# Kernel optimization log

Hardware: AMD Instinct MI355X
Metric: run time of the kernel (lower is better)

The kernel has to match this reference:

```python
import jax, jax.numpy as jnp
import numpy as np

B, H, W, C = 2, 64, 64, 96
DIN, NST, RNK, K = 192, 16, 6, 4
L = H * W


def _make_ids():
    idx = np.arange(L).reshape(H, W)
    p0 = idx.reshape(-1)
    p1 = idx.T.reshape(-1)
    p2 = p0[::-1].copy()
    p3 = p1[::-1].copy()
    scan = np.stack([p0, p1, p2, p3]).astype(np.int32)
    inv = np.stack([np.argsort(p) for p in scan]).astype(np.int32)
    return jnp.asarray(scan), jnp.asarray(inv)


def setup_inputs() -> dict:
    key = jax.random.key(0)
    ks = jax.random.split(key, 10)
    scan_ids, inv_ids = _make_ids()
    std = RNK ** -0.5
    # dt bias init: inverse-softplus of dt ~ LogUniform(1e-3, 1e-1), as in VMM.dt_init
    u = jax.random.uniform(ks[5], (K, DIN))
    dt = jnp.exp(u * (np.log(0.1) - np.log(0.001)) + np.log(0.001))
    dt_b = dt + jnp.log(-jnp.expm1(-dt))
    return {
        "x": jax.random.normal(ks[0], (B, H, W, C), jnp.float32),
        "W_in": jax.random.normal(ks[1], (2 * DIN, C), jnp.float32) * 0.02,
        "conv_w": jax.random.normal(ks[2], (DIN, 1, 3, 3), jnp.float32) * 0.1,
        "conv_b": jnp.zeros((DIN,), jnp.float32),
        "x_proj_w": jax.random.normal(ks[3], (K, RNK + 2 * NST, DIN), jnp.float32) * 0.02,
        "dt_w": jax.random.uniform(ks[4], (K, DIN, RNK), jnp.float32, -std, std),
        "dt_b": dt_b.astype(jnp.float32),
        "A_logs": jnp.log(jnp.tile(jnp.arange(1, NST + 1, dtype=jnp.float32)[None], (K * DIN, 1))),
        "Ds": jnp.ones((K * DIN,), jnp.float32),
        "gate_w": jax.random.normal(ks[6], (4 * DIN, 4), jnp.float32) * 0.1,  # grouped 1x1 conv, groups=DIN
        "gate_b": jnp.zeros((4 * DIN,), jnp.float32),
        "ln_g": jnp.ones((DIN,), jnp.float32),
        "ln_b": jnp.zeros((DIN,), jnp.float32),
        "W_out": jax.random.normal(ks[7], (C, DIN), jnp.float32) * 0.02,
        "scan_ids": scan_ids,
        "inv_ids": inv_ids,
    }


def _forward(x, W_in, conv_w, conv_b, x_proj_w, dt_w, dt_b, A_logs, Ds, gate_w, gate_b, ln_g, ln_b, W_out, scan_ids, inv_ids):
    b, h, w, c = x.shape
    l = h * w
    din = conv_w.shape[0]
    k = x_proj_w.shape[0]
    nst = A_logs.shape[1]
    rnk = dt_w.shape[2]
    # in_proj + split into x / gate z
    xz = x @ W_in.T
    xc, z = jnp.split(xz, 2, axis=-1)
    xc = jnp.transpose(xc, (0, 3, 1, 2))  # (b, din, h, w)
    # depthwise 3x3 conv + SiLU
    xc = jax.lax.conv_general_dilated(
        xc, conv_w, (1, 1), "SAME", feature_group_count=din,
        dimension_numbers=("NCHW", "OIHW", "NCHW")) + conv_b[None, :, None, None]
    xc = jax.nn.silu(xc)
    # multi-directional gather (mair_ids_scan)
    xf = xc.reshape(b, din, l)
    xs = jnp.moveaxis(xf[:, :, scan_ids], 2, 1)  # (b, k, din, l)
    # x_proj (grouped 1x1 conv) -> dt, B, C
    x_dbl = jnp.einsum("bkdl,krd->bkrl", xs, x_proj_w)
    dts, Bs, Cs = jnp.split(x_dbl, [rnk, rnk + nst], axis=2)  # (b,k,rnk,l),(b,k,n,l),(b,k,n,l)
    delta = jax.nn.softplus(jnp.einsum("bkrl,kdr->bkdl", dts, dt_w) + dt_b[None, :, :, None])
    A = -jnp.exp(A_logs).reshape(k, din, nst)
    dA = jnp.exp(delta[..., None] * A[None, :, :, None, :])              # (b,k,d,l,n)
    dBu = (delta * xs)[..., None] * jnp.moveaxis(Bs, 2, 3)[:, :, None]   # (b,k,d,l,n)

    def step(hst, inp):
        da, dbu = inp
        hst = da * hst + dbu
        return hst, hst

    h0 = jnp.zeros((b, k, din, nst), jnp.float32)
    _, hs = jax.lax.scan(step, h0, (jnp.moveaxis(dA, 3, 0), jnp.moveaxis(dBu, 3, 0)))  # (l,b,k,d,n)
    ys = jnp.einsum("lbkdn,bknl->bkdl", hs, Cs) + xs * Ds.reshape(k, din)[None, :, :, None]
    # inverse scatter (mair_ids_inverse) + concat along channels
    y = jax.vmap(lambda yk, ik: yk[..., ik], in_axes=(1, 0), out_axes=1)(ys, inv_ids)
    y = y.reshape(b, k * din, h, w)
    # ShuffleAttn gating: group = din, group_channels = k
    shuf = y.reshape(b, k, din, h, w).transpose(0, 2, 1, 3, 4).reshape(b, k * din, h, w)
    pooled = shuf.mean(axis=(2, 3)).reshape(b, din, k)
    gate = jax.nn.sigmoid(jnp.einsum("bgi,goi->bgo", pooled, gate_w.reshape(din, k, k)) + gate_b.reshape(din, k))
    gate = gate.transpose(0, 2, 1).reshape(b, k * din)  # channel_rearrange
    y = y * gate[:, :, None, None]
    # sum the 4 direction branches
    y = y.reshape(b, k, din, h, w).sum(axis=1)
    y = jnp.transpose(y, (0, 2, 3, 1))  # (b,h,w,din)
    # LayerNorm(d_inner)
    mu = y.mean(-1, keepdims=True)
    var = ((y - mu) ** 2).mean(-1, keepdims=True)
    y = (y - mu) / jnp.sqrt(var + 1e-5) * ln_g + ln_b
    y = y * jax.nn.silu(z)
    return y @ W_out.T


def reference(x, W_in, conv_w, conv_b, x_proj_w, dt_w, dt_b, A_logs, Ds, gate_w, gate_b, ln_g, ln_b, W_out, scan_ids, inv_ids):
    return _forward(x, W_in, conv_w, conv_b, x_proj_w, dt_w, dt_b, A_logs, Ds, gate_w, gate_b, ln_g, ln_b, W_out, scan_ids, inv_ids)
```

## Files before the change

kernel.cpp:

```cpp
#include <hip/hip_runtime.h>
#include <math.h>

#define BB 2
#define CC 96
#define DIN 192
#define NST 16
#define RNK 6
#define KK 4
#define LL 4096
#define RTOT (RNK + 2*NST)


__global__ __launch_bounds__(256) void k_inproj(const float* __restrict__ x,
        const float* __restrict__ W_in, float* __restrict__ xc_pre,
        float* __restrict__ z_silu) {
    __shared__ float lx[96*65];
    __shared__ float wt[48*196];
    int b = blockIdx.y, z = blockIdx.z;
    int l0 = blockIdx.x * 64;
    int t = threadIdx.x;
    for (int i = 0; i < 24; ++i) {
        int e = t + 256*i;
        int l = e / 96, c = e % 96;
        lx[c*65 + l] = x[((size_t)(b*LL + l0 + l))*96 + c];
    }
    int lg = t & 15;
    int og = t >> 4;
    float acc[4][12];
    #pragma unroll
    for (int j = 0; j < 4; ++j)
        #pragma unroll
        for (int q = 0; q < 12; ++q) acc[j][q] = 0.f;
    for (int p = 0; p < 2; ++p) {
        __syncthreads();
        for (int i = 0; i < 36; ++i) {
            int e = t + 256*i;
            int cc = e % 48, oc = e / 48;
            wt[cc*196 + oc] = W_in[((size_t)(z*192 + oc))*96 + p*48 + cc];
        }
        __syncthreads();
        #pragma unroll 2
        for (int cc = 0; cc < 48; ++cc) {
            int c = p*48 + cc;
            float x0 = lx[c*65 + 4*lg + 0];
            float x1 = lx[c*65 + 4*lg + 1];
            float x2 = lx[c*65 + 4*lg + 2];
            float x3 = lx[c*65 + 4*lg + 3];
            const float* wr = &wt[cc*196 + 12*og];
            float4 w0 = *(const float4*)(wr);
            float4 w1 = *(const float4*)(wr + 4);
            float4 w2 = *(const float4*)(wr + 8);
            float wv[12] = {w0.x,w0.y,w0.z,w0.w, w1.x,w1.y,w1.z,w1.w,
                            w2.x,w2.y,w2.z,w2.w};
            #pragma unroll
            for (int q = 0; q < 12; ++q) {
                acc[0][q] += x0*wv[q];
                acc[1][q] += x1*wv[q];
                acc[2][q] += x2*wv[q];
                acc[3][q] += x3*wv[q];
            }
        }
    }
    float* dst = (z == 0) ? xc_pre : z_silu;
    #pragma unroll
    for (int j = 0; j < 4; ++j) {
        int l = l0 + 4*lg + j;
        size_t base = (size_t)(b*LL + l)*DIN + 12*og;
        #pragma unroll
        for (int q = 0; q < 12; ++q) {
            float v = acc[j][q];
            if (z) v = v / (1.f + __expf(-v));
            dst[base + q] = v;
        }
    }
}

__global__ __launch_bounds__(256) void k_conv(const float* __restrict__ xc,
        const float* __restrict__ cw, const float* __restrict__ cb,
        float* __restrict__ out) {
    int gid = blockIdx.x*256 + threadIdx.x;
    int d = gid % DIN;
    int r = gid / DIN;
    int l = r & 4095, b = r >> 12;
    int w = l & 63, h = l >> 6;
    float acc = cb[d];
    #pragma unroll
    for (int dh = -1; dh <= 1; ++dh) {
        int h2 = h + dh;
        bool okh = (h2 >= 0) && (h2 < 64);
        #pragma unroll
        for (int dw = -1; dw <= 1; ++dw) {
            int w2 = w + dw;
            if (okh && w2 >= 0 && w2 < 64)
                acc += xc[((size_t)(b*LL + h2*64 + w2))*DIN + d] * cw[d*9 + (dh+1)*3 + (dw+1)];
        }
    }
    out[((size_t)(b*LL + l))*DIN + d] = acc / (1.f + __expf(-acc));
}

__global__ __launch_bounds__(512) void k_proj(const float* __restrict__ xconv,
        const int* __restrict__ scan_ids,
        const float* __restrict__ xpw, const float* __restrict__ dtw,
        const float* __restrict__ dtb,
        float* __restrict__ Bs, float* __restrict__ Cs, float* __restrict__ delta) {
    __shared__ float lxs[DIN*65];
    __shared__ float lw[RTOT*DIN];
    __shared__ float lbc[64*33];
    __shared__ float ldts[RNK*64];
    __shared__ int lsid[64];
    int k = blockIdx.y, b = blockIdx.z;
    int l0 = blockIdx.x * 64;
    int t = threadIdx.x;
    if (t < 64) lsid[t] = scan_ids[k*LL + l0 + t];
    for (int i = 0; i < 15; ++i) {
        int e = t + 512*i;
        if (e < RTOT*DIN) lw[e] = xpw[(size_t)k*RTOT*DIN + e];
    }
    __syncthreads();
    for (int i = 0; i < 24; ++i) {
        int e = t + 512*i;
        int d = e % DIN, l = e / DIN;
        lxs[d*65 + l] = xconv[((size_t)(b*LL + lsid[l]))*DIN + d];
    }
    __syncthreads();
    int l = t & 63;
    int rg = __builtin_amdgcn_readfirstlane(t >> 6);
    float acc[5];
    #pragma unroll
    for (int j = 0; j < 5; ++j) acc[j] = 0.f;
    for (int d = 0; d < DIN; d += 4) {
        float x0 = lxs[(d+0)*65 + l];
        float x1 = lxs[(d+1)*65 + l];
        float x2 = lxs[(d+2)*65 + l];
        float x3 = lxs[(d+3)*65 + l];
        #pragma unroll
        for (int j = 0; j < 5; ++j) {
            int r = rg + 8*j;
            if (r < RTOT) {
                float4 w = *(const float4*)&lw[r*DIN + d];
                acc[j] += x0*w.x + x1*w.y + x2*w.z + x3*w.w;
            }
        }
    }
    #pragma unroll
    for (int j = 0; j < 5; ++j) {
        int r = rg + 8*j;
        if (r < RTOT) {
            if (r < RNK) ldts[r*64 + l] = acc[j];
            else         lbc[l*33 + (r - RNK)] = acc[j];
        }
    }
    __syncthreads();
    size_t rowb = ((size_t)((b*KK + k)*LL + l0))*NST;
    for (int i = 0; i < 2; ++i) {
        int e = t + 512*i;
        int n = e & 15, ll = e >> 4;
        Bs[rowb + ll*NST + n] = lbc[ll*33 + n];
        Cs[rowb + ll*NST + n] = lbc[ll*33 + 16 + n];
    }
    for (int i = 0; i < 24; ++i) {
        int e = t + 512*i;
        int d = e % DIN, ll = e / DIN;
        float a = dtb[k*DIN + d];
        #pragma unroll
        for (int r = 0; r < RNK; ++r)
            a += ldts[r*64 + ll] * dtw[(k*DIN + d)*RNK + r];
        float sp = fmaxf(a, 0.f) + __logf(1.f + __expf(-fabsf(a)));
        delta[((size_t)((b*KK + k)*LL + l0 + ll))*DIN + d] = sp;
    }
}

__global__ __launch_bounds__(192) void k_scan1(const float* __restrict__ delta,
        const float* __restrict__ xconv, const float* __restrict__ Bs,
        const int* __restrict__ scan_ids, const float* __restrict__ A_logs,
        float* __restrict__ segA, float* __restrict__ segB, int SL) {
    __shared__ int lsid[256];
    int seg = blockIdx.x, bk = blockIdx.y;
    int b = bk >> 2, k = bk & 3;
    int d = threadIdx.x;
    int l0 = seg * SL;
    for (int i = threadIdx.x; i < SL; i += 192) lsid[i] = scan_ids[k*LL + l0 + i];
    __syncthreads();
    float Av[16];
    {
        const float4* ap = (const float4*)(A_logs + (k*DIN + d)*NST);
        #pragma unroll
        for (int q = 0; q < 4; ++q) {
            float4 v = ap[q];
            Av[4*q+0] = -__expf(v.x); Av[4*q+1] = -__expf(v.y);
            Av[4*q+2] = -__expf(v.z); Av[4*q+3] = -__expf(v.w);
        }
    }
    float a[16], h[16];
    #pragma unroll
    for (int n = 0; n < 16; ++n) { a[n] = 1.f; h[n] = 0.f; }
    const float* dp = delta + ((size_t)bk*LL + l0)*DIN + d;
    const float4* bq = (const float4*)(Bs + ((size_t)bk*LL + l0)*NST);
    for (int li = 0; li < SL; ++li) {
        float dv = dp[(size_t)li*DIN];
        float xv = xconv[((size_t)(b*LL + lsid[li]))*DIN + d];
        float dxv = dv * xv;
        float bb[16];
        #pragma unroll
        for (int q = 0; q < 4; ++q) {
            float4 v = bq[li*4 + q];
            bb[4*q+0] = v.x; bb[4*q+1] = v.y; bb[4*q+2] = v.z; bb[4*q+3] = v.w;
        }
        #pragma unroll
        for (int n = 0; n < 16; ++n) {
            float e = __expf(dv * Av[n]);
            a[n] *= e;
            h[n] = e*h[n] + dxv*bb[n];
        }
    }
    float4* sa = (float4*)(segA + (((size_t)bk*gridDim.x + seg)*DIN + d)*NST);
    float4* sb = (float4*)(segB + (((size_t)bk*gridDim.x + seg)*DIN + d)*NST);
    #pragma unroll
    for (int q = 0; q < 4; ++q) {
        sa[q] = make_float4(a[4*q], a[4*q+1], a[4*q+2], a[4*q+3]);
        sb[q] = make_float4(h[4*q], h[4*q+1], h[4*q+2], h[4*q+3]);
    }
}

__global__ __launch_bounds__(256) void k_scan2(const float* __restrict__ segA,
        const float* __restrict__ segB, float* __restrict__ hinit, int SEGC) {
    int idx = blockIdx.x*256 + threadIdx.x;
    if (idx >= BB*KK*DIN*NST) return;
    int bk = idx / (DIN*NST);
    int dn = idx % (DIN*NST);
    float h = 0.f;
    for (int s = 0; s < SEGC; ++s) {
        size_t o = ((size_t)(bk*SEGC + s))*(DIN*NST) + dn;
        hinit[o] = h;
        h = segA[o]*h + segB[o];
    }
}

__global__ __launch_bounds__(192) void k_scan3(const float* __restrict__ delta,
        const float* __restrict__ xconv, const float* __restrict__ Bs,
        const float* __restrict__ Cs,
        const int* __restrict__ scan_ids, const float* __restrict__ A_logs,
        const float* __restrict__ Ds, const float* __restrict__ hinit,
        float* __restrict__ y_dirs, float* __restrict__ poolsum, int SL) {
    __shared__ int lsid[256];
    int seg = blockIdx.x, bk = blockIdx.y;
    int b = bk >> 2, k = bk & 3;
    int d = threadIdx.x;
    int l0 = seg * SL;
    for (int i = threadIdx.x; i < SL; i += 192) lsid[i] = scan_ids[k*LL + l0 + i];
    __syncthreads();
    float Av[16];
    {
        const float4* ap = (const float4*)(A_logs + (k*DIN + d)*NST);
        #pragma unroll
        for (int q = 0; q < 4; ++q) {
            float4 v = ap[q];
            Av[4*q+0] = -__expf(v.x); Av[4*q+1] = -__expf(v.y);
            Av[4*q+2] = -__expf(v.z); Av[4*q+3] = -__expf(v.w);
        }
    }
    float Dv = Ds[k*DIN + d];
    float h[16];
    {
        const float4* hp = (const float4*)(hinit + (((size_t)bk*gridDim.x + seg)*DIN + d)*NST);
        #pragma unroll
        for (int q = 0; q < 4; ++q) {
            float4 v = hp[q];
            h[4*q+0] = v.x; h[4*q+1] = v.y; h[4*q+2] = v.z; h[4*q+3] = v.w;
        }
    }
    const float* dp = delta + ((size_t)bk*LL + l0)*DIN + d;
    const float4* bq = (const float4*)(Bs + ((size_t)bk*LL + l0)*NST);
    const float4* cq = (const float4*)(Cs + ((size_t)bk*LL + l0)*NST);
    float pool = 0.f;
    for (int li = 0; li < SL; ++li) {
        float dv = dp[(size_t)li*DIN];
        int l = lsid[li];
        float xv = xconv[((size_t)(b*LL + l))*DIN + d];
        float dxv = dv * xv;
        float bb[16], cc[16];
        #pragma unroll
        for (int q = 0; q < 4; ++q) {
            float4 v = bq[li*4 + q];
            bb[4*q+0] = v.x; bb[4*q+1] = v.y; bb[4*q+2] = v.z; bb[4*q+3] = v.w;
            float4 u = cq[li*4 + q];
            cc[4*q+0] = u.x; cc[4*q+1] = u.y; cc[4*q+2] = u.z; cc[4*q+3] = u.w;
        }
        float y = 0.f;
        #pragma unroll
        for (int n = 0; n < 16; ++n) {
            float e = __expf(dv * Av[n]);
            h[n] = e*h[n] + dxv*bb[n];
            y += h[n]*cc[n];
        }
        y += xv * Dv;
        y_dirs[((size_t)(bk*LL + l))*DIN + d] = y;
        pool += y;
    }
    atomicAdd(&poolsum[(b*DIN + d)*KK + k], pool);
}

__global__ void k_gate(const float* __restrict__ poolsum, const float* __restrict__ gw,
        const float* __restrict__ gb, float* __restrict__ gate) {
    int idx = blockIdx.x*256 + threadIdx.x;
    int o = idx & 3;
    int bd = idx >> 2;
    int d = bd % DIN;
    float acc = gb[d*KK + o];
    #pragma unroll
    for (int i = 0; i < KK; ++i)
        acc += (poolsum[bd*KK + i] * (1.f/LL)) * gw[(d*KK + o)*KK + i];
    gate[idx] = 1.f/(1.f + __expf(-acc));
}

__global__ __launch_bounds__(256) void k_final(const float* __restrict__ y_dirs,
        const float* __restrict__ gate, const float* __restrict__ z_silu,
        const float* __restrict__ lng, const float* __restrict__ lnb,
        const float* __restrict__ Wout, float* __restrict__ out) {
    __shared__ float buf[16*193];
    __shared__ float lmu[16], lrs[16];
    int b = blockIdx.y;
    int l0 = blockIdx.x * 16;
    int t = threadIdx.x;
    for (int i = 0; i < 12; ++i) {
        int e = t + 256*i;
        int d = e % DIN, l = e / DIN;
        float acc = 0.f;
        #pragma unroll
        for (int k = 0; k < KK; ++k)
            acc += y_dirs[((size_t)((b*KK + k)*LL + l0 + l))*DIN + d] * gate[(b*DIN + d)*KK + k];
        buf[l*193 + d] = acc;
    }
    __syncthreads();
    int l2 = t >> 4, q = t & 15;
    float s = 0.f, s2 = 0.f;
    for (int i = 0; i < 12; ++i) {
        float v = buf[l2*193 + q + 16*i];
        s += v; s2 += v*v;
    }
    s += __shfl_xor(s, 1);  s2 += __shfl_xor(s2, 1);
    s += __shfl_xor(s, 2);  s2 += __shfl_xor(s2, 2);
    s += __shfl_xor(s, 4);  s2 += __shfl_xor(s2, 4);
    s += __shfl_xor(s, 8);  s2 += __shfl_xor(s2, 8);
    if (q == 0) {
        float mu = s * (1.f/DIN);
        float var = s2 * (1.f/DIN) - mu*mu;
        lmu[l2] = mu;
        lrs[l2] = rsqrtf(var + 1e-5f);
    }
    __syncthreads();
    for (int i = 0; i < 12; ++i) {
        int e = t + 256*i;
        int d = e % DIN, l = e / DIN;
        float v = buf[l*193 + d];
        float tv = (v - lmu[l]) * lrs[l] * lng[d] + lnb[d];
        tv *= z_silu[((size_t)(b*LL + l0 + l))*DIN + d];
        buf[l*193 + d] = tv;
    }
    __syncthreads();
    int l = t & 15;
    int c0 = (t >> 4) * 6;
    float acc[6];
    #pragma unroll
    for (int cc = 0; cc < 6; ++cc) acc[cc] = 0.f;
    for (int d = 0; d < DIN; ++d) {
        float v = buf[l*193 + d];
        #pragma unroll
        for (int cc = 0; cc < 6; ++cc)
            acc[cc] += v * Wout[(c0 + cc)*DIN + d];
    }
    #pragma unroll
    for (int cc = 0; cc < 6; ++cc)
        out[((size_t)(b*LL + l0 + l))*CC + c0 + cc] = acc[cc];
}

extern "C" void kernel_launch(void* const* d_in, const int* in_sizes, int n_in,
                              void* d_out, int out_size, void* d_ws, size_t ws_size,
                              hipStream_t stream) {
    const float* x      = (const float*)d_in[0];
    const float* W_in   = (const float*)d_in[1];
    const float* conv_w = (const float*)d_in[2];
    const float* conv_b = (const float*)d_in[3];
    const float* xpw    = (const float*)d_in[4];
    const float* dt_w   = (const float*)d_in[5];
    const float* dt_b   = (const float*)d_in[6];
    const float* A_logs = (const float*)d_in[7];
    const float* Ds     = (const float*)d_in[8];
    const float* gate_w = (const float*)d_in[9];
    const float* gate_b = (const float*)d_in[10];
    const float* ln_g   = (const float*)d_in[11];
    const float* ln_b   = (const float*)d_in[12];
    const float* W_out  = (const float*)d_in[13];
    const int* scan_ids = (const int*)d_in[14];
    float* out = (float*)d_out;

    const size_t baseF = 6291456ull  + 2ull*1572864
                       + 6291456ull  + 2ull*524288  + 3072;
    int SEGC = 16;
    if ((baseF + 3ull*128*24576)*4 <= ws_size) SEGC = 128;
    else if ((baseF + 3ull*64*24576)*4 <= ws_size) SEGC = 64;
    else if ((baseF + 3ull*32*24576)*4 <= ws_size) SEGC = 32;
    int SL = LL / SEGC;
    size_t segF = (size_t)SEGC * 24576;

    float* ws      = (float*)d_ws;
    float* y_dirs  = ws;
    float* xc_pre  = ws;
    float* z_silu  = y_dirs  + 6291456;
    float* xconv   = z_silu  + 1572864;
    float* delta   = xconv   + 1572864;
    float* Bs      = delta   + 6291456;
    float* Cs      = Bs      + 524288;
    float* poolsum = Cs      + 524288;
    float* gate    = poolsum + 1536;
    float* segA    = gate    + 1536;
    float* segB    = segA    + segF;
    float* hinit   = segB    + segF;

    hipMemsetAsync(poolsum, 0, 1536*sizeof(float), stream);

    k_inproj<<<dim3(LL/64, BB, 2), 256, 0, stream>>>(x, W_in, xc_pre, z_silu);
    k_conv<<<(BB*DIN*LL)/256, 256, 0, stream>>>(xc_pre, conv_w, conv_b, xconv);
    k_proj<<<dim3(LL/64, KK, BB), 512, 0, stream>>>(xconv, scan_ids, xpw, dt_w, dt_b,
                                                    Bs, Cs, delta);
    k_scan1<<<dim3(SEGC, BB*KK), 192, 0, stream>>>(delta, xconv, Bs, scan_ids,
                                                   A_logs, segA, segB, SL);
    k_scan2<<<(BB*KK*DIN*NST + 255)/256, 256, 0, stream>>>(segA, segB, hinit, SEGC);
    k_scan3<<<dim3(SEGC, BB*KK), 192, 0, stream>>>(delta, xconv, Bs, Cs, scan_ids,
                                                   A_logs, Ds, hinit, y_dirs, poolsum, SL);
    k_gate<<<(BB*DIN*KK)/256, 256, 0, stream>>>(poolsum, gate_w, gate_b, gate);
    k_final<<<dim3(LL/16, BB), 256, 0, stream>>>(y_dirs, gate, z_silu, ln_g, ln_b, W_out, out);
}
```

Measured before the change: 319.5 us.

## Fuse dt projection into scan kernels and split state dim across thread pairs

k_proj now writes only the low-rank dt values (6 per position), and k_scan1/k_scan3 recompute delta = softplus(dt_w·dts + b) per 32-step chunk into shared memory. This removes the large delta tensor and its write and re-read traffic. Each scan thread now handles 8 of the 16 state channels, using 384 threads per block, and the halves of y are combined with a shuffle. B/C are staged in LDS, xconv is prefetched one step ahead, and k_proj's LDS is halved by looping over two DIN halves. The cost is computing delta twice, once in each scan pass, and extra barriers per chunk.

```diff
diff --git a/kernel.cpp b/kernel.cpp
--- a/kernel.cpp
+++ b/kernel.cpp
@@ -99,127 +99,133 @@
 }
 
 __global__ __launch_bounds__(512) void k_proj(const float* __restrict__ xconv,
-        const int* __restrict__ scan_ids,
-        const float* __restrict__ xpw, const float* __restrict__ dtw,
-        const float* __restrict__ dtb,
-        float* __restrict__ Bs, float* __restrict__ Cs, float* __restrict__ delta) {
-    __shared__ float lxs[DIN*65];
-    __shared__ float lw[RTOT*DIN];
+        const int* __restrict__ scan_ids, const float* __restrict__ xpw,
+        float* __restrict__ dts, float* __restrict__ Bs, float* __restrict__ Cs) {
+    __shared__ float lxs[96*65];
+    __shared__ float lw[RTOT*96];
     __shared__ float lbc[64*33];
-    __shared__ float ldts[RNK*64];
     __shared__ int lsid[64];
     int k = blockIdx.y, b = blockIdx.z;
     int l0 = blockIdx.x * 64;
     int t = threadIdx.x;
     if (t < 64) lsid[t] = scan_ids[k*LL + l0 + t];
-    for (int i = 0; i < 15; ++i) {
-        int e = t + 512*i;
-        if (e < RTOT*DIN) lw[e] = xpw[(size_t)k*RTOT*DIN + e];
-    }
-    __syncthreads();
-    for (int i = 0; i < 24; ++i) {
-        int e = t + 512*i;
-        int d = e % DIN, l = e / DIN;
-        lxs[d*65 + l] = xconv[((size_t)(b*LL + lsid[l]))*DIN + d];
-    }
-    __syncthreads();
     int l = t & 63;
     int rg = __builtin_amdgcn_readfirstlane(t >> 6);
     float acc[5];
     #pragma unroll
     for (int j = 0; j < 5; ++j) acc[j] = 0.f;
-    for (int d = 0; d < DIN; d += 4) {
-        float x0 = lxs[(d+0)*65 + l];
-        float x1 = lxs[(d+1)*65 + l];
-        float x2 = lxs[(d+2)*65 + l];
-        float x3 = lxs[(d+3)*65 + l];
-        #pragma unroll
-        for (int j = 0; j < 5; ++j) {
-            int r = rg + 8*j;
-            if (r < RTOT) {
-                float4 w = *(const float4*)&lw[r*DIN + d];
-                acc[j] += x0*w.x + x1*w.y + x2*w.z + x3*w.w;
-            }
-        }
-    }
+    for (int p = 0; p < 2; ++p) {
+        __syncthreads();
+        for (int i = 0; i < 12; ++i) {
+            int e = t + 512*i;
+            int dd = e % 96, ll = e / 96;
+            lxs[dd*65 + ll] = xconv[((size_t)(b*LL + lsid[ll]))*DIN + p*96 + dd];
+        }
+        for (int i = 0; i < 8; ++i) {
+            int e = t + 512*i;
+            if (e < RTOT*96) {
+                int r = e / 96, dd = e % 96;
+                lw[r*96 + dd] = xpw[(size_t)k*RTOT*DIN + r*DIN + p*96 + dd];
+            }
+        }
+        __syncthreads();
+        for (int dd = 0; dd < 96; dd += 4) {
+            float x0 = lxs[(dd+0)*65 + l];
+            float x1 = lxs[(dd+1)*65 + l];
+            float x2 = lxs[(dd+2)*65 + l];
+            float x3 = lxs[(dd+3)*65 + l];
+            #pragma unroll
+            for (int j = 0; j < 5; ++j) {
+                int r = rg + 8*j;
+                if (r < RTOT) {
+                    float4 w = *(const float4*)&lw[r*96 + dd];
+                    acc[j] += x0*w.x + x1*w.y + x2*w.z + x3*w.w;
+                }
+            }
+        }
+    }
+    int bk = b*KK + k;
     #pragma unroll
     for (int j = 0; j < 5; ++j) {
         int r = rg + 8*j;
-        if (r < RTOT) {
-            if (r < RNK) ldts[r*64 + l] = acc[j];
-            else         lbc[l*33 + (r - RNK)] = acc[j];
-        }
-    }
-    __syncthreads();
-    size_t rowb = ((size_t)((b*KK + k)*LL + l0))*NST;
+        if (r < RNK)       dts[((size_t)bk*LL + l0 + l)*8 + r] = acc[j];
+        else if (r < RTOT) lbc[l*33 + (r - RNK)] = acc[j];
+    }
+    __syncthreads();
+    size_t rowb = ((size_t)bk*LL + l0)*NST;
     for (int i = 0; i < 2; ++i) {
         int e = t + 512*i;
         int n = e & 15, ll = e >> 4;
         Bs[rowb + ll*NST + n] = lbc[ll*33 + n];
         Cs[rowb + ll*NST + n] = lbc[ll*33 + 16 + n];
     }
-    for (int i = 0; i < 24; ++i) {
-        int e = t + 512*i;
-        int d = e % DIN, ll = e / DIN;
-        float a = dtb[k*DIN + d];
-        #pragma unroll
-        for (int r = 0; r < RNK; ++r)
-            a += ldts[r*64 + ll] * dtw[(k*DIN + d)*RNK + r];
-        float sp = fmaxf(a, 0.f) + __logf(1.f + __expf(-fabsf(a)));
-        delta[((size_t)((b*KK + k)*LL + l0 + ll))*DIN + d] = sp;
-    }
-}
-
-__global__ __launch_bounds__(192) void k_scan1(const float* __restrict__ delta,
-        const float* __restrict__ xconv, const float* __restrict__ Bs,
+}
+
+__global__ __launch_bounds__(384) void k_scan1(const float* __restrict__ xconv,
+        const float* __restrict__ Bs, const float* __restrict__ dts,
+        const float* __restrict__ dtw, const float* __restrict__ dtb,
         const int* __restrict__ scan_ids, const float* __restrict__ A_logs,
         float* __restrict__ segA, float* __restrict__ segB, int SL) {
+    __shared__ float ldel[32*DIN];
+    __shared__ float lB[32*NST];
     __shared__ int lsid[256];
     int seg = blockIdx.x, bk = blockIdx.y;
     int b = bk >> 2, k = bk & 3;
-    int d = threadIdx.x;
+    int t = threadIdx.x;
+    int half = t & 1, d = t >> 1;
     int l0 = seg * SL;
-    for (int i = threadIdx.x; i < SL; i += 192) lsid[i] = scan_ids[k*LL + l0 + i];
-    __syncthreads();
-    float Av[16];
+    for (int i = t; i < SL; i += 384) lsid[i] = scan_ids[k*LL + l0 + i];
+    float Av[8];
     {
-        const float4* ap = (const float4*)(A_logs + (k*DIN + d)*NST);
-        #pragma unroll
-        for (int q = 0; q < 4; ++q) {
-            float4 v = ap[q];
-            Av[4*q+0] = -__expf(v.x); Av[4*q+1] = -__expf(v.y);
-            Av[4*q+2] = -__expf(v.z); Av[4*q+3] = -__expf(v.w);
-        }
-    }
-    float a[16], h[16];
-    #pragma unroll
-    for (int n = 0; n < 16; ++n) { a[n] = 1.f; h[n] = 0.f; }
-    const float* dp = delta + ((size_t)bk*LL + l0)*DIN + d;
-    const float4* bq = (const float4*)(Bs + ((size_t)bk*LL + l0)*NST);
-    for (int li = 0; li < SL; ++li) {
-        float dv = dp[(size_t)li*DIN];
-        float xv = xconv[((size_t)(b*LL + lsid[li]))*DIN + d];
-        float dxv = dv * xv;
-        float bb[16];
-        #pragma unroll
-        for (int q = 0; q < 4; ++q) {
-            float4 v = bq[li*4 + q];
-            bb[4*q+0] = v.x; bb[4*q+1] = v.y; bb[4*q+2] = v.z; bb[4*q+3] = v.w;
-        }
-        #pragma unroll
-        for (int n = 0; n < 16; ++n) {
-            float e = __expf(dv * Av[n]);
-            a[n] *= e;
-            h[n] = e*h[n] + dxv*bb[n];
-        }
-    }
-    float4* sa = (float4*)(segA + (((size_t)bk*gridDim.x + seg)*DIN + d)*NST);
-    float4* sb = (float4*)(segB + (((size_t)bk*gridDim.x + seg)*DIN + d)*NST);
-    #pragma unroll
-    for (int q = 0; q < 4; ++q) {
-        sa[q] = make_float4(a[4*q], a[4*q+1], a[4*q+2], a[4*q+3]);
-        sb[q] = make_float4(h[4*q], h[4*q+1], h[4*q+2], h[4*q+3]);
-    }
+        const float4* ap = (const float4*)(A_logs + ((k*DIN + d)*NST + half*8));
+        float4 a0 = ap[0], a1 = ap[1];
+        Av[0]=-__expf(a0.x); Av[1]=-__expf(a0.y); Av[2]=-__expf(a0.z); Av[3]=-__expf(a0.w);
+        Av[4]=-__expf(a1.x); Av[5]=-__expf(a1.y); Av[6]=-__expf(a1.z); Av[7]=-__expf(a1.w);
+    }
+    int dd = t % DIN, li0 = t / DIN;
+    float wdt[RNK];
+    float bdt = dtb[k*DIN + dd];
+    #pragma unroll
+    for (int r = 0; r < RNK; ++r) wdt[r] = dtw[(k*DIN + dd)*RNK + r];
+    float a[8], h[8];
+    #pragma unroll
+    for (int n = 0; n < 8; ++n) { a[n] = 1.f; h[n] = 0.f; }
+    __syncthreads();
+    float xn = xconv[((size_t)(b*LL + lsid[0]))*DIN + d];
+    for (int c0 = 0; c0 < SL; c0 += 32) {
+        for (int li = li0; li < 32; li += 2) {
+            const float* dr = dts + ((size_t)bk*LL + l0 + c0 + li)*8;
+            float aa = bdt;
+            #pragma unroll
+            for (int r = 0; r < RNK; ++r) aa += dr[r]*wdt[r];
+            ldel[li*DIN + dd] = fmaxf(aa, 0.f) + __logf(1.f + __expf(-fabsf(aa)));
+        }
+        for (int e = t; e < 32*NST; e += 384)
+            lB[e] = Bs[((size_t)bk*LL + l0 + c0)*NST + e];
+        __syncthreads();
+        for (int li2 = 0; li2 < 32; ++li2) {
+            int li = c0 + li2;
+            float xv = xn;
+            if (li + 1 < SL) xn = xconv[((size_t)(b*LL + lsid[li+1]))*DIN + d];
+            float dv = ldel[li2*DIN + d];
+            float dxv = dv * xv;
+            float4 b0 = *(const float4*)&lB[li2*NST + half*8];
+            float4 b1 = *(const float4*)&lB[li2*NST + half*8 + 4];
+            float bb[8] = {b0.x,b0.y,b0.z,b0.w, b1.x,b1.y,b1.z,b1.w};
+            #pragma unroll
+            for (int n = 0; n < 8; ++n) {
+                float e2 = __expf(dv * Av[n]);
+                a[n] *= e2;
+                h[n] = e2*h[n] + dxv*bb[n];
+            }
+        }
+        __syncthreads();
+    }
+    size_t base = (((size_t)bk*gridDim.x + seg)*DIN + d)*NST + half*8;
+    *(float4*)&segA[base]     = make_float4(a[0],a[1],a[2],a[3]);
+    *(float4*)&segA[base + 4] = make_float4(a[4],a[5],a[6],a[7]);
+    *(float4*)&segB[base]     = make_float4(h[0],h[1],h[2],h[3]);
+    *(float4*)&segB[base + 4] = make_float4(h[4],h[5],h[6],h[7]);
 }
 
 __global__ __launch_bounds__(256) void k_scan2(const float* __restrict__ segA,
@@ -229,6 +235,7 @@
     int bk = idx / (DIN*NST);
     int dn = idx % (DIN*NST);
     float h = 0.f;
+    #pragma unroll 4
     for (int s = 0; s < SEGC; ++s) {
         size_t o = ((size_t)(bk*SEGC + s))*(DIN*NST) + dn;
         hinit[o] = h;
@@ -236,68 +243,90 @@
     }
 }
 
-__global__ __launch_bounds__(192) void k_scan3(const float* __restrict__ delta,
-        const float* __restrict__ xconv, const float* __restrict__ Bs,
-        const float* __restrict__ Cs,
+__global__ __launch_bounds__(384) void k_scan3(const float* __restrict__ xconv,
+        const float* __restrict__ Bs, const float* __restrict__ Cs,
+        const float* __restrict__ dts, const float* __restrict__ dtw,
+        const float* __restrict__ dtb,
         const int* __restrict__ scan_ids, const float* __restrict__ A_logs,
         const float* __restrict__ Ds, const float* __restrict__ hinit,
         float* __restrict__ y_dirs, float* __restrict__ poolsum, int SL) {
+    __shared__ float ldel[32*DIN];
+    __shared__ float lB[32*NST];
+    __shared__ float lC[32*NST];
     __shared__ int lsid[256];
     int seg = blockIdx.x, bk = blockIdx.y;
     int b = bk >> 2, k = bk & 3;
-    int d = threadIdx.x;
+    int t = threadIdx.x;
+    int half = t & 1, d = t >> 1;
     int l0 = seg * SL;
-    for (int i = threadIdx.x; i < SL; i += 192) lsid[i] = scan_ids[k*LL + l0 + i];
-    __syncthreads();
-    float Av[16];
+    for (int i = t; i < SL; i += 384) lsid[i] = scan_ids[k*LL + l0 + i];
+    float Av[8];
     {
-        const float4* ap = (const float4*)(A_logs + (k*DIN + d)*NST);
-        #pragma unroll
-        for (int q = 0; q < 4; ++q) {
-            float4 v = ap[q];
-            Av[4*q+0] = -__expf(v.x); Av[4*q+1] = -__expf(v.y);
-            Av[4*q+2] = -__expf(v.z); Av[4*q+3] = -__expf(v.w);
-        }
+        const float4* ap = (const float4*)(A_logs + ((k*DIN + d)*NST + half*8));
+        float4 a0 = ap[0], a1 = ap[1];
+        Av[0]=-__expf(a0.x); Av[1]=-__expf(a0.y); Av[2]=-__expf(a0.z); Av[3]=-__expf(a0.w);
+        Av[4]=-__expf(a1.x); Av[5]=-__expf(a1.y); Av[6]=-__expf(a1.z); Av[7]=-__expf(a1.w);
     }
     float Dv = Ds[k*DIN + d];
-    float h[16];
+    int dd = t % DIN, li0 = t / DIN;
+    float wdt[RNK];
+    float bdt = dtb[k*DIN + dd];
+    #pragma unroll
+    for (int r = 0; r < RNK; ++r) wdt[r] = dtw[(k*DIN + dd)*RNK + r];
+    float h[8];
     {
-        const float4* hp = (const float4*)(hinit + (((size_t)bk*gridDim.x + seg)*DIN + d)*NST);
-        #pragma unroll
-        for (int q = 0; q < 4; ++q) {
-            float4 v = hp[q];
-            h[4*q+0] = v.x; h[4*q+1] = v.y; h[4*q+2] = v.z; h[4*q+3] = v.w;
-        }
-    }
-    const float* dp = delta + ((size_t)bk*LL + l0)*DIN + d;
-    const float4* bq = (const float4*)(Bs + ((size_t)bk*LL + l0)*NST);
-    const float4* cq = (const float4*)(Cs + ((size_t)bk*LL + l0)*NST);
+        size_t base = (((size_t)bk*gridDim.x + seg)*DIN + d)*NST + half*8;
+        float4 h0 = *(const float4*)&hinit[base];
+        float4 h1 = *(const float4*)&hinit[base + 4];
+        h[0]=h0.x; h[1]=h0.y; h[2]=h0.z; h[3]=h0.w;
+        h[4]=h1.x; h[5]=h1.y; h[6]=h1.z; h[7]=h1.w;
+    }
+    __syncthreads();
+    float xn = xconv[((size_t)(b*LL + lsid[0]))*DIN + d];
     float pool = 0.f;
-    for (int li = 0; li < SL; ++li) {
-        float dv = dp[(size_t)li*DIN];
-        int l = lsid[li];
-        float xv = xconv[((size_t)(b*LL + l))*DIN + d];
-        float dxv = dv * xv;
-        float bb[16], cc[16];
-        #pragma unroll
-        for (int q = 0; q < 4; ++q) {
-            float4 v = bq[li*4 + q];
-            bb[4*q+0] = v.x; bb[4*q+1] = v.y; bb[4*q+2] = v.z; bb[4*q+3] = v.w;
-            float4 u = cq[li*4 + q];
-            cc[4*q+0] = u.x; cc[4*q+1] = u.y; cc[4*q+2] = u.z; cc[4*q+3] = u.w;
-        }
-        float y = 0.f;
-        #pragma unroll
-        for (int n = 0; n < 16; ++n) {
-            float e = __expf(dv * Av[n]);
-            h[n] = e*h[n] + dxv*bb[n];
-            y += h[n]*cc[n];
-        }
-        y += xv * Dv;
-        y_dirs[((size_t)(bk*LL + l))*DIN + d] = y;
-        pool += y;
-    }
-    atomicAdd(&poolsum[(b*DIN + d)*KK + k], pool);
+    for (int c0 = 0; c0 < SL; c0 += 32) {
+        for (int li = li0; li < 32; li += 2) {
+            const float* dr = dts + ((size_t)bk*LL + l0 + c0 + li)*8;
+            float aa = bdt;
+            #pragma unroll
+            for (int r = 0; r < RNK; ++r) aa += dr[r]*wdt[r];
+            ldel[li*DIN + dd] = fmaxf(aa, 0.f) + __logf(1.f + __expf(-fabsf(aa)));
+        }
+        for (int e = t; e < 32*NST; e += 384) {
+            lB[e] = Bs[((size_t)bk*LL + l0 + c0)*NST + e];
+            lC[e] = Cs[((size_t)bk*LL + l0 + c0)*NST + e];
+        }
+        __syncthreads();
+        for (int li2 = 0; li2 < 32; ++li2) {
+            int li = c0 + li2;
+            int l = lsid[li];
+            float xv = xn;
+            if (li + 1 < SL) xn = xconv[((size_t)(b*LL + lsid[li+1]))*DIN + d];
+            float dv = ldel[li2*DIN + d];
+            float dxv = dv * xv;
+            float4 b0 = *(const float4*)&lB[li2*NST + half*8];
+            float4 b1 = *(const float4*)&lB[li2*NST + half*8 + 4];
+            float4 c0v = *(const float4*)&lC[li2*NST + half*8];
+            float4 c1v = *(const float4*)&lC[li2*NST + half*8 + 4];
+            float bb[8] = {b0.x,b0.y,b0.z,b0.w, b1.x,b1.y,b1.z,b1.w};
+            float cc[8] = {c0v.x,c0v.y,c0v.z,c0v.w, c1v.x,c1v.y,c1v.z,c1v.w};
+            float y = 0.f;
+            #pragma unroll
+            for (int n = 0; n < 8; ++n) {
+                float e2 = __expf(dv * Av[n]);
+                h[n] = e2*h[n] + dxv*bb[n];
+                y += h[n]*cc[n];
+            }
+            y += __shfl_xor(y, 1);
+            if (half == 0) {
+                y += xv * Dv;
+                y_dirs[((size_t)(bk*LL + l))*DIN + d] = y;
+                pool += y;
+            }
+        }
+        __syncthreads();
+    }
+    if (half == 0) atomicAdd(&poolsum[(b*DIN + d)*KK + k], pool);
 }
 
 __global__ void k_gate(const float* __restrict__ poolsum, const float* __restrict__ gw,
@@ -394,8 +423,7 @@
     const int* scan_ids = (const int*)d_in[14];
     float* out = (float*)d_out;
 
-    const size_t baseF = 6291456ull  + 2ull*1572864
-                       + 6291456ull  + 2ull*524288  + 3072;
+    const size_t baseF = 6291456ull + 2ull*1572864 + 262144ull + 2ull*524288 + 3072;
     int SEGC = 16;
     if ((baseF + 3ull*128*24576)*4 <= ws_size) SEGC = 128;
     else if ((baseF + 3ull*64*24576)*4 <= ws_size) SEGC = 64;
@@ -408,8 +436,8 @@
     float* xc_pre  = ws;
     float* z_silu  = y_dirs  + 6291456;
     float* xconv   = z_silu  + 1572864;
-    float* delta   = xconv   + 1572864;
-    float* Bs      = delta   + 6291456;
+    float* dts     = xconv   + 1572864;
+    float* Bs      = dts     + 262144;
     float* Cs      = Bs      + 524288;
     float* poolsum = Cs      + 524288;
     float* gate    = poolsum + 1536;
@@ -421,13 +449,14 @@
 
     k_inproj<<<dim3(LL/64, BB, 2), 256, 0, stream>>>(x, W_in, xc_pre, z_silu);
     k_conv<<<(BB*DIN*LL)/256, 256, 0, stream>>>(xc_pre, conv_w, conv_b, xconv);
-    k_proj<<<dim3(LL/64, KK, BB), 512, 0, stream>>>(xconv, scan_ids, xpw, dt_w, dt_b,
-                                                    Bs, Cs, delta);
-    k_scan1<<<dim3(SEGC, BB*KK), 192, 0, stream>>>(delta, xconv, Bs, scan_ids,
-                                                   A_logs, segA, segB, SL);
+    k_proj<<<dim3(LL/64, KK, BB), 512, 0, stream>>>(xconv, scan_ids, xpw,
+                                                    dts, Bs, Cs);
+    k_scan1<<<dim3(SEGC, BB*KK), 384, 0, stream>>>(xconv, Bs, dts, dt_w, dt_b,
+                                                   scan_ids, A_logs, segA, segB, SL);
     k_scan2<<<(BB*KK*DIN*NST + 255)/256, 256, 0, stream>>>(segA, segB, hinit, SEGC);
-    k_scan3<<<dim3(SEGC, BB*KK), 192, 0, stream>>>(delta, xconv, Bs, Cs, scan_ids,
-                                                   A_logs, Ds, hinit, y_dirs, poolsum, SL);
+    k_scan3<<<dim3(SEGC, BB*KK), 384, 0, stream>>>(xconv, Bs, Cs, dts, dt_w, dt_b,
+                                                   scan_ids, A_logs, Ds, hinit,
+                                                   y_dirs, poolsum, SL);
     k_gate<<<(BB*DIN*KK)/256, 256, 0, stream>>>(poolsum, gate_w, gate_b, gate);
     k_final<<<dim3(LL/16, BB), 256, 0, stream>>>(y_dirs, gate, z_silu, ln_g, ln_b, W_out, out);
 }
```

Result: faster. 284.2 us (-11.0%).
